# Optimization experiments

Measured on AMD Instinct MI355X. Metric: run time of the kernel, lower is better.

Reference implementation:

```python
import jax, jax.numpy as jnp
import numpy as np

N = 100000      # nodes
E = 1600000     # edges (avg degree 16)
IN_DIM = 64
OUT_DIM = 128
BN_EPS = 1e-5


def setup_inputs() -> dict:
    key = jax.random.key(0)
    kx, ke, kw, kb, ks = jax.random.split(key, 5)
    x = jax.random.normal(kx, (N, IN_DIM), dtype=jnp.float32)
    edge_index = jax.random.randint(ke, (2, E), 0, N, dtype=jnp.int32)
    # GCNConv linear weight (no bias inside lin; conv bias separate)
    W = jax.random.normal(kw, (IN_DIM, OUT_DIM), dtype=jnp.float32) / np.sqrt(IN_DIM)
    bias = jax.random.normal(kb, (OUT_DIM,), dtype=jnp.float32) * 0.01
    # skip projection Linear(in_dim, out_dim, bias=False)
    skip_W = jax.random.normal(ks, (IN_DIM, OUT_DIM), dtype=jnp.float32) / np.sqrt(IN_DIM)
    # BatchNorm1d affine params (training-mode batch stats used in forward)
    gamma = jnp.ones((OUT_DIM,), dtype=jnp.float32)
    beta = jnp.zeros((OUT_DIM,), dtype=jnp.float32)
    return {"x": x, "edge_index": edge_index, "W": W, "bias": bias,
            "skip_W": skip_W, "gamma": gamma, "beta": beta}


def _gcn_forward(x, edge_index, W, bias, skip_W, gamma, beta):
    n = x.shape[0]
    # GCNConv, normalize=True, add_self_loops=True (PyG defaults)
    row, col = edge_index[0], edge_index[1]
    loop = jnp.arange(n, dtype=edge_index.dtype)
    row_f = jnp.concatenate([row, loop])   # source nodes
    col_f = jnp.concatenate([col, loop])   # target nodes

    xt = x @ W                             # [N, OUT]
    deg = jax.ops.segment_sum(jnp.ones_like(col_f, dtype=xt.dtype), col_f,
                              num_segments=n)          # >= 1 due to self loops
    dinv = jax.lax.rsqrt(deg)
    norm = dinv[row_f] * dinv[col_f]                    # [E+N]
    msgs = xt[row_f] * norm[:, None]                    # gather + scale
    out = jax.ops.segment_sum(msgs, col_f, num_segments=n) + bias

    # skip-sum (in_dim != out_dim -> project)
    out = out + x @ skip_W

    # BatchNorm1d (training-mode batch statistics), affine
    mean = out.mean(axis=0)
    var = out.var(axis=0)
    out = (out - mean) * jax.lax.rsqrt(var + BN_EPS) * gamma + beta

    # ReLU; dropout p=0.0 -> identity
    return jax.nn.relu(out)


def reference(x, edge_index, W, bias, skip_W, gamma, beta):
    return _gcn_forward(x, edge_index, W, bias, skip_W, gamma, beta)
```

## Files before the change

kernel.cpp:

```cpp
#include <hip/hip_runtime.h>


typedef unsigned short ushort;
typedef __bf16 bf16x8 __attribute__((ext_vector_type(8)));
typedef float f32x4 __attribute__((ext_vector_type(4)));
typedef float f32x2 __attribute__((ext_vector_type(2)));
typedef ushort u16x8 __attribute__((ext_vector_type(8)));

constexpr int N_NODES = 100000;
constexpr int N_PAD   = 100096;
constexpr int E_EDGES = 1600000;

constexpr int BUCK_SHIFT = 7;
constexpr int NBUCK   = (N_NODES + 127) / 128;
constexpr int NBUCK_P = 784;
constexpr int CHUNK   = 8192;
constexpr int NCHUNK  = (E_EDGES + CHUNK - 1) / CHUNK;
constexpr int GH_STRIDE = 200;
constexpr int SORT_CAP = 4096;

constexpr size_t OFF_SCALE  = 0;
constexpr size_t OFF_DINV   = 256;
constexpr size_t OFF_ROWPTR = 100352;
constexpr size_t OFF_BASE   = 200480;
constexpr size_t OFF_GHIST  = 201280;
constexpr size_t OFF_BINNED = 358080;
constexpr size_t OFF_U      = 1958080;
constexpr size_t OFF_PRE    = 5161152;
constexpr size_t OFF_XD8    = OFF_PRE;
constexpr size_t OFF_BT     = 11567296;
constexpr size_t OFF_GSUM   = 11575488;
constexpr size_t OFF_TICK   = 11575744;

static __device__ __forceinline__ ushort f2bf(float f) {
    union { float f; unsigned u; } v; v.f = f;
    unsigned r = v.u + 0x7FFFu + ((v.u >> 16) & 1u);
    return (ushort)(r >> 16);
}
static __device__ __forceinline__ float bf2f(ushort u) {
    union { unsigned u; float f; } v; v.u = (unsigned)u << 16;
    return v.f;
}
static __device__ __forceinline__ unsigned pack_fp8x4(float a, float b, float c, float d) {
    int r = 0;
    r = __builtin_amdgcn_cvt_pk_fp8_f32(a, b, r, false);
    r = __builtin_amdgcn_cvt_pk_fp8_f32(c, d, r, true);
    return (unsigned)r;
}
static __device__ __forceinline__ bf16x8 pack_bf8(float4 a, float4 b) {
    union { ushort us[8]; bf16x8 v; } u;
    u.us[0] = f2bf(a.x); u.us[1] = f2bf(a.y); u.us[2] = f2bf(a.z); u.us[3] = f2bf(a.w);
    u.us[4] = f2bf(b.x); u.us[5] = f2bf(b.y); u.us[6] = f2bf(b.z); u.us[7] = f2bf(b.w);
    return u.v;
}

__global__ __launch_bounds__(256) void k_hist(const int* __restrict__ col,
                                              int* __restrict__ gh_t,
                                              const float* __restrict__ W,
                                              const float* __restrict__ skipW,
                                              ushort* __restrict__ Bt,
                                              float* __restrict__ gsum,
                                              unsigned* __restrict__ tick) {
    int c = blockIdx.x, t = threadIdx.x;
    if (c >= NCHUNK) {
        int idx = (c - NCHUNK) * 256 + t;
        if (c == NCHUNK) {
            gsum[t] = 0.f;
            if (t < 2) tick[t] = 0u;
        }
        int k = idx >> 7, n = idx & 127;
        float v = (k < 64) ? W[k * 128 + n] : skipW[(k - 64) * 128 + n];
        Bt[n * 128 + k] = f2bf(v);
        return;
    }
    __shared__ int h[NBUCK_P];
    for (int b = t; b < NBUCK_P; b += 256) h[b] = 0;
    __syncthreads();
    const int4* col4 = (const int4*)col;
    int g0 = c * (CHUNK / 4);
#pragma unroll
    for (int i = 0; i < CHUNK / 1024; ++i) {
        int g4 = g0 + i * 256 + t;
        if (g4 * 4 + 3 < E_EDGES) {
            int4 cc = col4[g4];
            atomicAdd(&h[cc.x >> BUCK_SHIFT], 1);
            atomicAdd(&h[cc.y >> BUCK_SHIFT], 1);
            atomicAdd(&h[cc.z >> BUCK_SHIFT], 1);
            atomicAdd(&h[cc.w >> BUCK_SHIFT], 1);
        } else {
#pragma unroll
            for (int j = 0; j < 4; ++j) {
                int e = g4 * 4 + j;
                if (e < E_EDGES) atomicAdd(&h[col[e] >> BUCK_SHIFT], 1);
            }
        }
    }
    __syncthreads();
    for (int b = t; b < NBUCK_P; b += 256) gh_t[(size_t)b * GH_STRIDE + c] = h[b];
}

__global__ __launch_bounds__(256) void k_scan(int* __restrict__ gh_t,
                                              int* __restrict__ base,
                                              int* __restrict__ rowptr,
                                              unsigned* __restrict__ tick) {
    __shared__ int wtot[4];
    __shared__ int amlast;
    int w = threadIdx.x >> 6, l = threadIdx.x & 63;
    int b = blockIdx.x * 4 + w;
    int* rowp = gh_t + (size_t)b * GH_STRIDE;
    int carry = 0;
#pragma unroll
    for (int i = 0; i < 4; ++i) {
        int idx = i * 64 + l;
        int v = (idx < NCHUNK) ? rowp[idx] : 0;
        int orig = v;
#pragma unroll
        for (int d = 1; d < 64; d <<= 1) {
            int o = __shfl_up(v, d);
            if (l >= d) v += o;
        }
        if (idx < NCHUNK) rowp[idx] = carry + v - orig;
        carry += __shfl(v, 63);
    }
    if (l == 0 && b < NBUCK) atomicExch(&base[b], carry);
    __syncthreads();
    if (threadIdx.x == 0)
        amlast = (atomicAdd(tick + 0, 1u) == (unsigned)(gridDim.x - 1)) ? 1 : 0;
    __syncthreads();
    if (!amlast) return;

    int t = threadIdx.x;
    int i0 = t * 4;
    int v0 = (i0 + 0 < NBUCK) ? atomicAdd(&base[i0 + 0], 0) : 0;
    int v1 = (i0 + 1 < NBUCK) ? atomicAdd(&base[i0 + 1], 0) : 0;
    int v2 = (i0 + 2 < NBUCK) ? atomicAdd(&base[i0 + 2], 0) : 0;
    int v3 = (i0 + 3 < NBUCK) ? atomicAdd(&base[i0 + 3], 0) : 0;
    int s = v0 + v1 + v2 + v3;
    int incl = s;
#pragma unroll
    for (int d = 1; d < 64; d <<= 1) {
        int o = __shfl_up(incl, d);
        if (l >= d) incl += o;
    }
    if (l == 63) wtot[w] = incl;
    __syncthreads();
    int wpre = 0;
    for (int ww = 0; ww < w; ++ww) wpre += wtot[ww];
    int excl = wpre + incl - s;
    if (i0 + 0 < NBUCK) base[i0 + 0] = excl;
    if (i0 + 1 < NBUCK) base[i0 + 1] = excl + v0;
    if (i0 + 2 < NBUCK) base[i0 + 2] = excl + v0 + v1;
    if (i0 + 3 < NBUCK) base[i0 + 3] = excl + v0 + v1 + v2;
    if (t == 255) {
        int total = wpre + incl;
        base[NBUCK] = total;
        rowptr[N_NODES] = total;
    }
}

__global__ __launch_bounds__(256) void k_scatter_bin(const int* __restrict__ row,
                                                     const int* __restrict__ col,
                                                     const int* __restrict__ gh_t,
                                                     const int* __restrict__ base,
                                                     unsigned int* __restrict__ binned) {
    __shared__ int cur[NBUCK_P];
    int c = blockIdx.x, t = threadIdx.x;
    for (int b = t; b < NBUCK_P; b += 256) {
        int bb = (b < NBUCK) ? base[b] : 0;
        cur[b] = bb + gh_t[(size_t)b * GH_STRIDE + c];
    }
    __syncthreads();
    const int4* col4 = (const int4*)col;
    const int4* row4 = (const int4*)row;
    int g0 = c * (CHUNK / 4);
#pragma unroll
    for (int i = 0; i < CHUNK / 1024; ++i) {
        int g4 = g0 + i * 256 + t;
        if (g4 * 4 + 3 < E_EDGES) {
            int4 cc = col4[g4];
            int4 rr = row4[g4];
            int p;
            p = atomicAdd(&cur[cc.x >> BUCK_SHIFT], 1);
            binned[p] = ((unsigned)(cc.x & 127) << 17) | (unsigned)rr.x;
            p = atomicAdd(&cur[cc.y >> BUCK_SHIFT], 1);
            binned[p] = ((unsigned)(cc.y & 127) << 17) | (unsigned)rr.y;
            p = atomicAdd(&cur[cc.z >> BUCK_SHIFT], 1);
            binned[p] = ((unsigned)(cc.z & 127) << 17) | (unsigned)rr.z;
            p = atomicAdd(&cur[cc.w >> BUCK_SHIFT], 1);
            binned[p] = ((unsigned)(cc.w & 127) << 17) | (unsigned)rr.w;
        } else {
#pragma unroll
            for (int j = 0; j < 4; ++j) {
                int e = g4 * 4 + j;
                if (e < E_EDGES) {
                    int d = col[e], s = row[e];
                    int p = atomicAdd(&cur[d >> BUCK_SHIFT], 1);
                    binned[p] = ((unsigned)(d & 127) << 17) | (unsigned)s;
                }
            }
        }
    }
}

__global__ __launch_bounds__(256) void k_sortbucket(unsigned int* __restrict__ binned,
                                                    const int* __restrict__ base,
                                                    int* __restrict__ rowptr,
                                                    float* __restrict__ dinv,
                                                    const float* __restrict__ x,
                                                    unsigned* __restrict__ xd8) {
    __shared__ unsigned int ebuf[SORT_CAP];
    __shared__ int sbuf[SORT_CAP];
    __shared__ int lcnt[128];
    __shared__ int lptr[128];
    __shared__ float ldinv[128];
    __shared__ int wsum[2];
    int b = blockIdx.x, t = threadIdx.x;
    int i0 = base[b], i1 = base[b + 1];
    int cnt = i1 - i0;
    if (cnt > SORT_CAP) cnt = SORT_CAP;
    int n0 = b << BUCK_SHIFT;
    int nn = min(128, N_NODES - n0);

    for (int k = t; k < cnt; k += 256) ebuf[k] = binned[i0 + k];
    if (t < 128) lcnt[t] = 0;
    __syncthreads();
    for (int k = t; k < cnt; k += 256) atomicAdd(&lcnt[ebuf[k] >> 17], 1);
    __syncthreads();

    int myc = 0, val = 0;
    if (t < 128) {
        myc = lcnt[t];
        val = myc;
#pragma unroll
        for (int d = 1; d < 64; d <<= 1) {
            int o = __shfl_up(val, d);
            if ((t & 63) >= d) val += o;
        }
        if ((t & 63) == 63) wsum[t >> 6] = val;
    }
    __syncthreads();
    if (t < 128) {
        if (t >= 64) val += wsum[0];
        int excl = val - myc;
        lptr[t] = excl;
        float dv = rsqrtf((float)myc + 1.0f);
        ldinv[t] = dv;
        if (t < nn) {
            rowptr[n0 + t] = i0 + excl;
            dinv[n0 + t] = dv;
        }
    }
    __syncthreads();
    for (int k = t; k < cnt; k += 256) {
        unsigned int e = ebuf[k];
        int j = (int)(e >> 17);
        int p = atomicAdd(&lptr[j], 1);
        sbuf[p] = (int)(e & 0x1FFFF);
    }
    __syncthreads();
    for (int k = t; k < cnt; k += 256) binned[i0 + k] = (unsigned int)sbuf[k];

#pragma unroll
    for (int it = 0; it < 8; ++it) {
        int idx = it * 256 + t;
        int nl = idx >> 4, q = idx & 15;
        int c = n0 + nl;
        unsigned w8 = 0;
        if (nl < nn) {
            float4 v = ((const float4*)x)[(size_t)c * 16 + q];
            float d = ldinv[nl];
            w8 = pack_fp8x4(v.x * d, v.y * d, v.z * d, v.w * d);
        }
        xd8[(size_t)c * 16 + q] = w8;
    }
}

__global__ __launch_bounds__(256) void k_agg(const unsigned* __restrict__ xd8,
                                             const float* __restrict__ dinv,
                                             const int* __restrict__ rowptr,
                                             const unsigned int* __restrict__ csr,
                                             ushort* __restrict__ u) {
    int t = blockIdx.x * blockDim.x + threadIdx.x;
    if (t >= N_PAD * 16) return;
    int c = t >> 4;
    int q = t & 15;
    if (c >= N_NODES) {
        ushort4 z = {0, 0, 0, 0};
        ((ushort4*)u)[t] = z;
        return;
    }
    float dc = dinv[c];
    float4 acc;
    {
        unsigned w = xd8[t];
        f32x2 lo = __builtin_amdgcn_cvt_pk_f32_fp8((int)w, false);
        f32x2 hi = __builtin_amdgcn_cvt_pk_f32_fp8((int)w, true);
        acc.x = lo.x; acc.y = lo.y; acc.z = hi.x; acc.w = hi.y;
    }
    int i0 = rowptr[c], i1 = rowptr[c + 1];
    int i = i0;
    for (; i + 8 <= i1; i += 8) {
        int s[8];
#pragma unroll
        for (int k = 0; k < 8; ++k) s[k] = (int)csr[i + k];
        unsigned w[8];
#pragma unroll
        for (int k = 0; k < 8; ++k) w[k] = xd8[s[k] * 16 + q];
#pragma unroll
        for (int k = 0; k < 8; ++k) {
            f32x2 lo = __builtin_amdgcn_cvt_pk_f32_fp8((int)w[k], false);
            f32x2 hi = __builtin_amdgcn_cvt_pk_f32_fp8((int)w[k], true);
            acc.x += lo.x; acc.y += lo.y; acc.z += hi.x; acc.w += hi.y;
        }
    }
    for (; i < i1; ++i) {
        unsigned w = xd8[(int)csr[i] * 16 + q];
        f32x2 lo = __builtin_amdgcn_cvt_pk_f32_fp8((int)w, false);
        f32x2 hi = __builtin_amdgcn_cvt_pk_f32_fp8((int)w, true);
        acc.x += lo.x; acc.y += lo.y; acc.z += hi.x; acc.w += hi.y;
    }
    ushort4 o;
    o.x = f2bf(acc.x * dc); o.y = f2bf(acc.y * dc);
    o.z = f2bf(acc.z * dc); o.w = f2bf(acc.w * dc);
    ((ushort4*)u)[t] = o;
}

__global__ __launch_bounds__(256) void k_gemm(const ushort* __restrict__ u,
                                              const float* __restrict__ x,
                                              const ushort* __restrict__ Bt,
                                              const float* __restrict__ bias,
                                              ushort* __restrict__ pre,
                                              float* __restrict__ gsum,
                                              unsigned* __restrict__ tick,
                                              const float* __restrict__ gamma,
                                              const float* __restrict__ beta,
                                              float* __restrict__ scaleshift) {
    __shared__ float sred[128];
    __shared__ float qred[128];
    __shared__ int amlast;
    int tid = threadIdx.x;
    int wave = tid >> 6, lane = tid & 63;
    int wm = wave >> 1, wn = wave & 1;
    int l15 = lane & 15, quad = lane >> 4;
    int row0 = blockIdx.x * 128 + wm * 64;
    int col0 = wn * 64;

    if (tid < 128) { sred[tid] = 0.f; qred[tid] = 0.f; }
    __syncthreads();

    bf16x8 af[4][4], bf_[4][4];
#pragma unroll
    for (int kc = 0; kc < 2; ++kc) {
        int ko = kc * 32 + quad * 8;
#pragma unroll
        for (int im = 0; im < 4; ++im)
            af[kc][im] = *(const bf16x8*)&u[(size_t)(row0 + im * 16 + l15) * 64 + ko];
    }
#pragma unroll
    for (int kc = 2; kc < 4; ++kc) {
        int ko = (kc - 2) * 32 + quad * 8;
#pragma unroll
        for (int im = 0; im < 4; ++im) {
            int r = row0 + im * 16 + l15;
            float4 v0 = make_float4(0.f, 0.f, 0.f, 0.f);
            float4 v1 = v0;
            if (r < N_NODES) {
                v0 = *(const float4*)&x[(size_t)r * 64 + ko];
                v1 = *(const float4*)&x[(size_t)r * 64 + ko + 4];
            }
            af[kc][im] = pack_bf8(v0, v1);
        }
    }
#pragma unroll
    for (int kc = 0; kc < 4; ++kc)
#pragma unroll
        for (int jn = 0; jn < 4; ++jn)
            bf_[kc][jn] = *(const bf16x8*)&Bt[(size_t)(col0 + jn * 16 + l15) * 128 + kc * 32 + quad * 8];

    f32x4 acc[4][4];
#pragma unroll
    for (int a = 0; a < 4; ++a)
#pragma unroll
        for (int b = 0; b < 4; ++b) acc[a][b] = (f32x4){0.f, 0.f, 0.f, 0.f};

#pragma unroll
    for (int kc = 0; kc < 4; ++kc)
#pragma unroll
        for (int im = 0; im < 4; ++im)
#pragma unroll
            for (int jn = 0; jn < 4; ++jn)
                acc[im][jn] = __builtin_amdgcn_mfma_f32_16x16x32_bf16(
                    af[kc][im], bf_[kc][jn], acc[im][jn], 0, 0, 0);

    int coln[4];
    float bi[4];
#pragma unroll
    for (int jn = 0; jn < 4; ++jn) {
        coln[jn] = col0 + jn * 16 + l15;
        bi[jn] = bias[coln[jn]];
    }
    float lsum[4] = {0.f, 0.f, 0.f, 0.f};
    float lsq[4]  = {0.f, 0.f, 0.f, 0.f};
#pragma unroll
    for (int im = 0; im < 4; ++im) {
        int rbase = row0 + im * 16 + quad * 4;
#pragma unroll
        for (int r = 0; r < 4; ++r) {
            int rowi = rbase + r;
            if (rowi < N_NODES) {
#pragma unroll
                for (int jn = 0; jn < 4; ++jn) {
                    float v = acc[im][jn][r] + bi[jn];
                    pre[(size_t)rowi * 128 + coln[jn]] = f2bf(v);
                    lsum[jn] += v;
                    lsq[jn]  += v * v;
                }
            }
        }
    }
#pragma unroll
    for (int jn = 0; jn < 4; ++jn) {
        atomicAdd(&sred[coln[jn]], lsum[jn]);
        atomicAdd(&qred[coln[jn]], lsq[jn]);
    }
    __syncthreads();
    if (tid < 128) {
        atomicAdd(&gsum[tid], sred[tid]);
        atomicAdd(&gsum[128 + tid], qred[tid]);
    }
    __syncthreads();
    if (tid == 0)
        amlast = (atomicAdd(tick + 1, 1u) == (unsigned)(gridDim.x - 1)) ? 1 : 0;
    __syncthreads();
    if (amlast && tid < 128) {
        float s = atomicAdd(&gsum[tid], 0.f);
        float q = atomicAdd(&gsum[128 + tid], 0.f);
        float mean = s * (1.0f / N_NODES);
        float var  = q * (1.0f / N_NODES) - mean * mean;
        float sc   = gamma[tid] * rsqrtf(var + 1e-5f);
        scaleshift[tid]       = sc;
        scaleshift[128 + tid] = beta[tid] - mean * sc;
    }
}

__global__ __launch_bounds__(256) void k_apply(const ushort* __restrict__ pre,
                                               float* __restrict__ out,
                                               const float* __restrict__ ss) {
    int t = blockIdx.x * blockDim.x + threadIdx.x;
    if (t >= N_NODES * 16) return;
    int j8 = t & 15;
    u16x8 p = ((const u16x8*)pre)[t];
    float4 sc0 = ((const float4*)ss)[j8 * 2];
    float4 sc1 = ((const float4*)ss)[j8 * 2 + 1];
    float4 sh0 = ((const float4*)(ss + 128))[j8 * 2];
    float4 sh1 = ((const float4*)(ss + 128))[j8 * 2 + 1];
    float4 v0, v1;
    v0.x = fmaxf(fmaf(bf2f(p[0]), sc0.x, sh0.x), 0.f);
    v0.y = fmaxf(fmaf(bf2f(p[1]), sc0.y, sh0.y), 0.f);
    v0.z = fmaxf(fmaf(bf2f(p[2]), sc0.z, sh0.z), 0.f);
    v0.w = fmaxf(fmaf(bf2f(p[3]), sc0.w, sh0.w), 0.f);
    v1.x = fmaxf(fmaf(bf2f(p[4]), sc1.x, sh1.x), 0.f);
    v1.y = fmaxf(fmaf(bf2f(p[5]), sc1.y, sh1.y), 0.f);
    v1.z = fmaxf(fmaf(bf2f(p[6]), sc1.z, sh1.z), 0.f);
    v1.w = fmaxf(fmaf(bf2f(p[7]), sc1.w, sh1.w), 0.f);
    ((float4*)out)[t * 2]     = v0;
    ((float4*)out)[t * 2 + 1] = v1;
}

extern "C" void kernel_launch(void* const* d_in, const int* in_sizes, int n_in,
                              void* d_out, int out_size, void* d_ws, size_t ws_size,
                              hipStream_t stream) {
    const float* x      = (const float*)d_in[0];
    const int*   eidx   = (const int*)d_in[1];
    const float* W      = (const float*)d_in[2];
    const float* bias   = (const float*)d_in[3];
    const float* skipW  = (const float*)d_in[4];
    const float* gamma  = (const float*)d_in[5];
    const float* beta   = (const float*)d_in[6];
    float* out = (float*)d_out;
    float* ws  = (float*)d_ws;

    const int* row = eidx;
    const int* col = eidx + E_EDGES;

    float* scaleshift = ws + OFF_SCALE;
    float* dinv       = ws + OFF_DINV;
    int*   rowptr     = (int*)(ws + OFF_ROWPTR);
    int*   base       = (int*)(ws + OFF_BASE);
    int*   gh_t       = (int*)(ws + OFF_GHIST);
    unsigned int* binned = (unsigned int*)(ws + OFF_BINNED);
    ushort* u         = (ushort*)(ws + OFF_U);
    unsigned* xd8     = (unsigned*)(ws + OFF_XD8);
    ushort* pre       = (ushort*)(ws + OFF_PRE);
    ushort* Bt        = (ushort*)(ws + OFF_BT);
    float* gsum       = ws + OFF_GSUM;
    unsigned* tick    = (unsigned*)(ws + OFF_TICK);

    k_hist<<<NCHUNK + 64, 256, 0, stream>>>(col, gh_t, W, skipW, Bt, gsum, tick);
    k_scan<<<NBUCK_P / 4, 256, 0, stream>>>(gh_t, base, rowptr, tick);
    k_scatter_bin<<<NCHUNK, 256, 0, stream>>>(row, col, gh_t, base, binned);
    k_sortbucket<<<NBUCK, 256, 0, stream>>>(binned, base, rowptr, dinv, x, xd8);
    k_agg<<<(N_PAD * 16 + 255) / 256, 256, 0, stream>>>(xd8, dinv, rowptr, binned, u);
    k_gemm<<<NBUCK, 256, 0, stream>>>(u, x, Bt, bias, pre, gsum, tick, gamma, beta, scaleshift);
    k_apply<<<(N_NODES * 16 + 255) / 256, 256, 0, stream>>>(pre, out, scaleshift);
}
```

Before: 217.2 us.

## Concatenate aggregated and bf16 x rows into one A matrix; deterministic BN stat reduce

The sort-bucket kernel now writes a bf16 copy of x next to the aggregated features, giving one interleaved 128-wide A matrix. The GEMM can then load all four K-chunks with plain bf16 vector loads instead of converting fp32 x inside the GEMM. The GEMM now runs 512 threads per block, each wave covering a 64x32 tile, and writes per-block BN partial sums to a buffer. A new small reduce kernel replaces the global atomics and last-block ticket for the statistics, at the cost of an extra launch and extra bf16 x traffic.

Result: no change. 215.2 us (-0.9%).

```diff
diff --git a/kernel.cpp b/kernel.cpp
--- a/kernel.cpp
+++ b/kernel.cpp
@@ -25,12 +25,12 @@
 constexpr size_t OFF_BASE   = 200480;
 constexpr size_t OFF_GHIST  = 201280;
 constexpr size_t OFF_BINNED = 358080;
-constexpr size_t OFF_U      = 1958080;
-constexpr size_t OFF_PRE    = 5161152;
+constexpr size_t OFF_PART   = OFF_BINNED;
+constexpr size_t OFF_A      = 1958080;
+constexpr size_t OFF_PRE    = 8364224;
 constexpr size_t OFF_XD8    = OFF_PRE;
-constexpr size_t OFF_BT     = 11567296;
-constexpr size_t OFF_GSUM   = 11575488;
-constexpr size_t OFF_TICK   = 11575744;
+constexpr size_t OFF_BT     = 14770368;
+constexpr size_t OFF_TICK   = 14778560;
 
 static __device__ __forceinline__ ushort f2bf(float f) {
     union { float f; unsigned u; } v; v.f = f;
@@ -47,27 +47,17 @@
     r = __builtin_amdgcn_cvt_pk_fp8_f32(c, d, r, true);
     return (unsigned)r;
 }
-static __device__ __forceinline__ bf16x8 pack_bf8(float4 a, float4 b) {
-    union { ushort us[8]; bf16x8 v; } u;
-    u.us[0] = f2bf(a.x); u.us[1] = f2bf(a.y); u.us[2] = f2bf(a.z); u.us[3] = f2bf(a.w);
-    u.us[4] = f2bf(b.x); u.us[5] = f2bf(b.y); u.us[6] = f2bf(b.z); u.us[7] = f2bf(b.w);
-    return u.v;
-}
 
 __global__ __launch_bounds__(256) void k_hist(const int* __restrict__ col,
                                               int* __restrict__ gh_t,
                                               const float* __restrict__ W,
                                               const float* __restrict__ skipW,
                                               ushort* __restrict__ Bt,
-                                              float* __restrict__ gsum,
                                               unsigned* __restrict__ tick) {
     int c = blockIdx.x, t = threadIdx.x;
     if (c >= NCHUNK) {
         int idx = (c - NCHUNK) * 256 + t;
-        if (c == NCHUNK) {
-            gsum[t] = 0.f;
-            if (t < 2) tick[t] = 0u;
-        }
+        if (c == NCHUNK && t < 2) tick[t] = 0u;
         int k = idx >> 7, n = idx & 127;
         float v = (k < 64) ? W[k * 128 + n] : skipW[(k - 64) * 128 + n];
         Bt[n * 128 + k] = f2bf(v);
@@ -207,7 +197,8 @@
                                                     int* __restrict__ rowptr,
                                                     float* __restrict__ dinv,
                                                     const float* __restrict__ x,
-                                                    unsigned* __restrict__ xd8) {
+                                                    unsigned* __restrict__ xd8,
+                                                    ushort* __restrict__ A) {
     __shared__ unsigned int ebuf[SORT_CAP];
     __shared__ int sbuf[SORT_CAP];
     __shared__ int lcnt[128];
@@ -266,12 +257,15 @@
         int nl = idx >> 4, q = idx & 15;
         int c = n0 + nl;
         unsigned w8 = 0;
+        ushort4 xb = {0, 0, 0, 0};
         if (nl < nn) {
             float4 v = ((const float4*)x)[(size_t)c * 16 + q];
             float d = ldinv[nl];
             w8 = pack_fp8x4(v.x * d, v.y * d, v.z * d, v.w * d);
+            xb.x = f2bf(v.x); xb.y = f2bf(v.y); xb.z = f2bf(v.z); xb.w = f2bf(v.w);
         }
         xd8[(size_t)c * 16 + q] = w8;
+        ((ushort4*)A)[(size_t)c * 32 + 16 + q] = xb;
     }
 }
 
@@ -279,14 +273,14 @@
                                              const float* __restrict__ dinv,
                                              const int* __restrict__ rowptr,
                                              const unsigned int* __restrict__ csr,
-                                             ushort* __restrict__ u) {
+                                             ushort* __restrict__ A) {
     int t = blockIdx.x * blockDim.x + threadIdx.x;
     if (t >= N_PAD * 16) return;
     int c = t >> 4;
     int q = t & 15;
     if (c >= N_NODES) {
         ushort4 z = {0, 0, 0, 0};
-        ((ushort4*)u)[t] = z;
+        ((ushort4*)A)[(size_t)c * 32 + q] = z;
         return;
     }
     float dc = dinv[c];
@@ -322,85 +316,62 @@
     ushort4 o;
     o.x = f2bf(acc.x * dc); o.y = f2bf(acc.y * dc);
     o.z = f2bf(acc.z * dc); o.w = f2bf(acc.w * dc);
-    ((ushort4*)u)[t] = o;
-}
-
-__global__ __launch_bounds__(256) void k_gemm(const ushort* __restrict__ u,
-                                              const float* __restrict__ x,
+    ((ushort4*)A)[(size_t)c * 32 + q] = o;
+}
+
+__global__ __launch_bounds__(512) void k_gemm(const ushort* __restrict__ A,
                                               const ushort* __restrict__ Bt,
                                               const float* __restrict__ bias,
                                               ushort* __restrict__ pre,
-                                              float* __restrict__ gsum,
-                                              unsigned* __restrict__ tick,
-                                              const float* __restrict__ gamma,
-                                              const float* __restrict__ beta,
-                                              float* __restrict__ scaleshift) {
+                                              float* __restrict__ partial) {
     __shared__ float sred[128];
     __shared__ float qred[128];
-    __shared__ int amlast;
     int tid = threadIdx.x;
     int wave = tid >> 6, lane = tid & 63;
-    int wm = wave >> 1, wn = wave & 1;
+    int wm = wave >> 2, wn = wave & 3;
     int l15 = lane & 15, quad = lane >> 4;
     int row0 = blockIdx.x * 128 + wm * 64;
-    int col0 = wn * 64;
+    int col0 = wn * 32;
 
     if (tid < 128) { sred[tid] = 0.f; qred[tid] = 0.f; }
     __syncthreads();
 
-    bf16x8 af[4][4], bf_[4][4];
-#pragma unroll
-    for (int kc = 0; kc < 2; ++kc) {
+    bf16x8 af[4][4], bf_[4][2];
+#pragma unroll
+    for (int kc = 0; kc < 4; ++kc) {
         int ko = kc * 32 + quad * 8;
 #pragma unroll
         for (int im = 0; im < 4; ++im)
-            af[kc][im] = *(const bf16x8*)&u[(size_t)(row0 + im * 16 + l15) * 64 + ko];
-    }
-#pragma unroll
-    for (int kc = 2; kc < 4; ++kc) {
-        int ko = (kc - 2) * 32 + quad * 8;
-#pragma unroll
-        for (int im = 0; im < 4; ++im) {
-            int r = row0 + im * 16 + l15;
-            float4 v0 = make_float4(0.f, 0.f, 0.f, 0.f);
-            float4 v1 = v0;
-            if (r < N_NODES) {
-                v0 = *(const float4*)&x[(size_t)r * 64 + ko];
-                v1 = *(const float4*)&x[(size_t)r * 64 + ko + 4];
-            }
-            af[kc][im] = pack_bf8(v0, v1);
-        }
-    }
+            af[kc][im] = *(const bf16x8*)&A[(size_t)(row0 + im * 16 + l15) * 128 + ko];
+#pragma unroll
+        for (int jn = 0; jn < 2; ++jn)
+            bf_[kc][jn] = *(const bf16x8*)&Bt[(size_t)(col0 + jn * 16 + l15) * 128 + ko];
+    }
+
+    f32x4 acc[4][2];
+#pragma unroll
+    for (int a = 0; a < 4; ++a)
+#pragma unroll
+        for (int b = 0; b < 2; ++b) acc[a][b] = (f32x4){0.f, 0.f, 0.f, 0.f};
+
 #pragma unroll
     for (int kc = 0; kc < 4; ++kc)
 #pragma unroll
-        for (int jn = 0; jn < 4; ++jn)
-            bf_[kc][jn] = *(const bf16x8*)&Bt[(size_t)(col0 + jn * 16 + l15) * 128 + kc * 32 + quad * 8];
-
-    f32x4 acc[4][4];
-#pragma unroll
-    for (int a = 0; a < 4; ++a)
-#pragma unroll
-        for (int b = 0; b < 4; ++b) acc[a][b] = (f32x4){0.f, 0.f, 0.f, 0.f};
-
-#pragma unroll
-    for (int kc = 0; kc < 4; ++kc)
-#pragma unroll
         for (int im = 0; im < 4; ++im)
 #pragma unroll
-            for (int jn = 0; jn < 4; ++jn)
+            for (int jn = 0; jn < 2; ++jn)
                 acc[im][jn] = __builtin_amdgcn_mfma_f32_16x16x32_bf16(
                     af[kc][im], bf_[kc][jn], acc[im][jn], 0, 0, 0);
 
-    int coln[4];
-    float bi[4];
-#pragma unroll
-    for (int jn = 0; jn < 4; ++jn) {
+    int coln[2];
+    float bi[2];
+#pragma unroll
+    for (int jn = 0; jn < 2; ++jn) {
         coln[jn] = col0 + jn * 16 + l15;
         bi[jn] = bias[coln[jn]];
     }
-    float lsum[4] = {0.f, 0.f, 0.f, 0.f};
-    float lsq[4]  = {0.f, 0.f, 0.f, 0.f};
+    float lsum[2] = {0.f, 0.f};
+    float lsq[2]  = {0.f, 0.f};
 #pragma unroll
     for (int im = 0; im < 4; ++im) {
         int rbase = row0 + im * 16 + quad * 4;
@@ -409,7 +380,7 @@
             int rowi = rbase + r;
             if (rowi < N_NODES) {
 #pragma unroll
-                for (int jn = 0; jn < 4; ++jn) {
+                for (int jn = 0; jn < 2; ++jn) {
                     float v = acc[im][jn][r] + bi[jn];
                     pre[(size_t)rowi * 128 + coln[jn]] = f2bf(v);
                     lsum[jn] += v;
@@ -419,27 +390,42 @@
         }
     }
 #pragma unroll
-    for (int jn = 0; jn < 4; ++jn) {
+    for (int jn = 0; jn < 2; ++jn) {
         atomicAdd(&sred[coln[jn]], lsum[jn]);
         atomicAdd(&qred[coln[jn]], lsq[jn]);
     }
     __syncthreads();
     if (tid < 128) {
-        atomicAdd(&gsum[tid], sred[tid]);
-        atomicAdd(&gsum[128 + tid], qred[tid]);
-    }
-    __syncthreads();
-    if (tid == 0)
-        amlast = (atomicAdd(tick + 1, 1u) == (unsigned)(gridDim.x - 1)) ? 1 : 0;
-    __syncthreads();
-    if (amlast && tid < 128) {
-        float s = atomicAdd(&gsum[tid], 0.f);
-        float q = atomicAdd(&gsum[128 + tid], 0.f);
-        float mean = s * (1.0f / N_NODES);
-        float var  = q * (1.0f / N_NODES) - mean * mean;
-        float sc   = gamma[tid] * rsqrtf(var + 1e-5f);
-        scaleshift[tid]       = sc;
-        scaleshift[128 + tid] = beta[tid] - mean * sc;
+        partial[(size_t)blockIdx.x * 256 + tid]       = sred[tid];
+        partial[(size_t)blockIdx.x * 256 + 128 + tid] = qred[tid];
+    }
+}
+
+__global__ __launch_bounds__(256) void k_reduce(const float* __restrict__ partial,
+                                                const float* __restrict__ gamma,
+                                                const float* __restrict__ beta,
+                                                float* __restrict__ scaleshift) {
+    __shared__ float ls[256], lq[256];
+    int j = blockIdx.x;
+    int t = threadIdx.x;
+    float s = 0.f, q = 0.f;
+    for (int p = t; p < NBUCK; p += 256) {
+        s += partial[(size_t)p * 256 + j];
+        q += partial[(size_t)p * 256 + 128 + j];
+    }
+    ls[t] = s; lq[t] = q;
+    __syncthreads();
+#pragma unroll
+    for (int off = 128; off > 0; off >>= 1) {
+        if (t < off) { ls[t] += ls[t + off]; lq[t] += lq[t + off]; }
+        __syncthreads();
+    }
+    if (t == 0) {
+        float mean = ls[0] * (1.0f / N_NODES);
+        float var  = lq[0] * (1.0f / N_NODES) - mean * mean;
+        float sc   = gamma[j] * rsqrtf(var + 1e-5f);
+        scaleshift[j]       = sc;
+        scaleshift[128 + j] = beta[j] - mean * sc;
     }
 }
 
@@ -487,20 +473,21 @@
     float* dinv       = ws + OFF_DINV;
     int*   rowptr     = (int*)(ws + OFF_ROWPTR);
     int*   base       = (int*)(ws + OFF_BASE);
-    int*   gh_t       = (int*)(ws + OFF_GHIST);
+    int*   gh_t      = (int*)(ws + OFF_GHIST);
     unsigned int* binned = (unsigned int*)(ws + OFF_BINNED);
-    ushort* u         = (ushort*)(ws + OFF_U);
+    float* partial    = ws + OFF_PART;
+    ushort* A         = (ushort*)(ws + OFF_A);
     unsigned* xd8     = (unsigned*)(ws + OFF_XD8);
     ushort* pre       = (ushort*)(ws + OFF_PRE);
     ushort* Bt        = (ushort*)(ws + OFF_BT);
-    float* gsum       = ws + OFF_GSUM;
     unsigned* tick    = (unsigned*)(ws + OFF_TICK);
 
-    k_hist<<<NCHUNK + 64, 256, 0, stream>>>(col, gh_t, W, skipW, Bt, gsum, tick);
+    k_hist<<<NCHUNK + 64, 256, 0, stream>>>(col, gh_t, W, skipW, Bt, tick);
     k_scan<<<NBUCK_P / 4, 256, 0, stream>>>(gh_t, base, rowptr, tick);
     k_scatter_bin<<<NCHUNK, 256, 0, stream>>>(row, col, gh_t, base, binned);
-    k_sortbucket<<<NBUCK, 256, 0, stream>>>(binned, base, rowptr, dinv, x, xd8);
-    k_agg<<<(N_PAD * 16 + 255) / 256, 256, 0, stream>>>(xd8, dinv, rowptr, binned, u);
-    k_gemm<<<NBUCK, 256, 0, stream>>>(u, x, Bt, bias, pre, gsum, tick, gamma, beta, scaleshift);
+    k_sortbucket<<<NBUCK, 256, 0, stream>>>(binned, base, rowptr, dinv, x, xd8, A);
+    k_agg<<<(N_PAD * 16 + 255) / 256, 256, 0, stream>>>(xd8, dinv, rowptr, binned, A);
+    k_gemm<<<NBUCK, 512, 0, stream>>>(A, Bt, bias, pre, partial);
+    k_reduce<<<128, 256, 0, stream>>>(partial, gamma, beta, scaleshift);
     k_apply<<<(N_NODES * 16 + 255) / 256, 256, 0, stream>>>(pre, out, scaleshift);
 }
```
